# Kernel optimization log

Hardware: AMD Instinct MI355X
Metric: run time of the kernel (lower is better)

## Reference

```python
import jax, jax.numpy as jnp
import numpy as np

NUM_USERS = 100000
NUM_ITEMS = 100000
D = 64
L = 3
B = 4096
K = 50


def setup_inputs() -> dict:
    key = jax.random.key(0)
    ks = jax.random.split(key, 8)
    user_ids = jax.random.randint(ks[0], (B,), 0, NUM_USERS)
    item_ids = jax.random.randint(ks[1], (B,), 0, NUM_ITEMS)
    social_neighbors = jax.random.randint(ks[2], (B, K), 0, NUM_USERS)
    attention_mask = jax.random.uniform(ks[3], (B, K), dtype=jnp.float32)
    user_table = jax.random.normal(ks[4], (NUM_USERS, D), dtype=jnp.float32) * 0.1
    item_table = jax.random.normal(ks[5], (NUM_ITEMS, D), dtype=jnp.float32) * 0.1
    # xavier-ish scale for the square Linear layers
    Ws = jax.random.normal(ks[6], (L, D, D), dtype=jnp.float32) * (1.0 / np.sqrt(D))
    bs = jnp.zeros((L, D), dtype=jnp.float32)
    return {
        "user_ids": user_ids,
        "item_ids": item_ids,
        "social_neighbors": social_neighbors,
        "attention_mask": attention_mask,
        "user_table": user_table,
        "item_table": item_table,
        "Ws": Ws,
        "bs": bs,
    }


def reference(user_ids, item_ids, social_neighbors, attention_mask,
              user_table, item_table, Ws, bs):
    user_emb = user_table[user_ids]            # [B, D]
    item_emb = item_table[item_ids]            # [B, D]
    neighbor_emb = user_table[social_neighbors]  # [B, K, D]
    mask = attention_mask[..., None]           # [B, K, 1]
    for l in range(Ws.shape[0]):
        # faithful to original: mask is re-applied to neighbor_emb every layer
        neighbor_emb = neighbor_emb * mask
        neighbor_info = jnp.mean(neighbor_emb, axis=1)  # [B, D]
        # nn.Linear: x @ W.T + b
        user_emb = jax.nn.relu((user_emb + neighbor_info) @ Ws[l].T + bs[l])
    scores = user_emb @ item_emb.T              # [B, B]
    return scores
```

## Files before the change

kernel.cpp:

```cpp
#include <hip/hip_runtime.h>
#include <hip/hip_bf16.h>

#define BATCH 4096
#define DIM 64
#define KN 50
#define NL 3

typedef __attribute__((ext_vector_type(8))) short short8;
typedef __attribute__((ext_vector_type(4))) float f32x4;

__global__ __launch_bounds__(256) void rows_kernel(
    const int* __restrict__ user_ids,
    const int* __restrict__ item_ids,
    const int* __restrict__ nbrs,
    const float* __restrict__ mask,
    const float* __restrict__ user_table,
    const float* __restrict__ item_table,
    const float* __restrict__ Ws,
    const float* __restrict__ bs,
    __hip_bfloat16* __restrict__ Uout,
    __hip_bfloat16* __restrict__ Iout)
{
    __shared__ float Wlds[NL * 64 * 65];
    __shared__ float blds[NL * 64];
    __shared__ float xbuf[4][64];

    const int tid = threadIdx.x;

    for (int idx = tid; idx < NL * 64 * 64; idx += 256) {
        const int l = idx >> 12;
        const int rem = idx & 4095;
        const int j = rem >> 6;
        const int i = rem & 63;
        Wlds[l * (64 * 65) + j * 65 + i] = Ws[idx];
    }
    if (tid < NL * 64) blds[tid] = bs[tid];
    __syncthreads();

    const int wave = tid >> 6;
    const int lane = tid & 63;
    const int b = (blockIdx.x << 2) + wave;

    const int it = item_ids[b];
    Iout[b * DIM + lane] = __float2bfloat16(item_table[it * DIM + lane]);

    const int u = user_ids[b];
    float x = user_table[u * DIM + lane];

    int ni = 0;
    float wi = 0.0f;
    if (lane < KN) {
        ni = nbrs[b * KN + lane];
        wi = mask[b * KN + lane];
    }

    float acc1 = 0.f, acc2 = 0.f, acc3 = 0.f;
    #pragma unroll
    for (int k = 0; k < KN; ++k) {
        const int nk = __shfl(ni, k);
        const float wk = __shfl(wi, k);
        const float v = user_table[nk * DIM + lane];
        const float w2 = wk * wk;
        acc1 = fmaf(wk, v, acc1);
        acc2 = fmaf(w2, v, acc2);
        acc3 = fmaf(w2 * wk, v, acc3);
    }
    const float inv = 1.0f / (float)KN;
    const float nm0 = acc1 * inv, nm1 = acc2 * inv, nm2 = acc3 * inv;

    #pragma unroll
    for (int l = 0; l < NL; ++l) {
        const float nm = (l == 0) ? nm0 : (l == 1) ? nm1 : nm2;
        xbuf[wave][lane] = x + nm;
        float y = blds[l * 64 + lane];
        const float* wrow = &Wlds[l * (64 * 65) + lane * 65];
        #pragma unroll
        for (int i = 0; i < 64; ++i)
            y = fmaf(wrow[i], xbuf[wave][i], y);
        x = fmaxf(y, 0.0f);
    }
    Uout[b * DIM + lane] = __float2bfloat16(x);
}

__global__ __launch_bounds__(256) void scores_kernel(
    const __hip_bfloat16* __restrict__ U,
    const __hip_bfloat16* __restrict__ V,
    float* __restrict__ C)
{
    const int tid = threadIdx.x;
    const int wave = tid >> 6;
    const int lane = tid & 63;
    const int quad = lane >> 4;
    const int l16 = lane & 15;

    const int row0 = (blockIdx.y << 6) + (wave << 4);
    const int colG = blockIdx.x << 8;

    const short* Us = (const short*)U;
    const short* Vs = (const short*)V;

    const short* up = Us + (row0 + l16) * DIM + quad * 8;
    const short8 u0 = *(const short8*)(up);
    const short8 u1 = *(const short8*)(up + 32);

    #pragma unroll 4
    for (int ct = 0; ct < 16; ++ct) {
        const int col0 = colG + (ct << 4);
        const short* vp = Vs + (col0 + l16) * DIM + quad * 8;
        const short8 v0 = *(const short8*)(vp);
        const short8 v1 = *(const short8*)(vp + 32);
        f32x4 acc = {0.f, 0.f, 0.f, 0.f};
        acc = __builtin_amdgcn_mfma_f32_16x16x32_bf16(v0, u0, acc, 0, 0, 0);
        acc = __builtin_amdgcn_mfma_f32_16x16x32_bf16(v1, u1, acc, 0, 0, 0);
        float* cp = C + (size_t)(row0 + l16) * BATCH + col0 + (quad << 2);
        *(float4*)cp = make_float4(acc[0], acc[1], acc[2], acc[3]);
    }
}

extern "C" void kernel_launch(void* const* d_in, const int* in_sizes, int n_in,
                              void* d_out, int out_size, void* d_ws, size_t ws_size,
                              hipStream_t stream)
{
    const int* user_ids   = (const int*)d_in[0];
    const int* item_ids   = (const int*)d_in[1];
    const int* nbrs       = (const int*)d_in[2];
    const float* mask     = (const float*)d_in[3];
    const float* utable   = (const float*)d_in[4];
    const float* itable   = (const float*)d_in[5];
    const float* Ws       = (const float*)d_in[6];
    const float* bs       = (const float*)d_in[7];
    float* out = (float*)d_out;

    __hip_bfloat16* Ubf = (__hip_bfloat16*)d_ws;
    __hip_bfloat16* Ibf = Ubf + BATCH * DIM;

    rows_kernel<<<BATCH / 4, 256, 0, stream>>>(user_ids, item_ids, nbrs, mask,
                                               utable, itable, Ws, bs, Ubf, Ibf);
    scores_kernel<<<dim3(16, 64), 256, 0, stream>>>(Ubf, Ibf, out);
}
```

Baseline: 142.2 us.

## Split gather from MLP and amortize weight LDS loads over four rows

Measured after the change: 139.8 us. Within noise of the previous version (-1.7%).

```diff
diff --git a/kernel.cpp b/kernel.cpp
--- a/kernel.cpp
+++ b/kernel.cpp
@@ -9,21 +9,60 @@
 typedef __attribute__((ext_vector_type(8))) short short8;
 typedef __attribute__((ext_vector_type(4))) float f32x4;
 
-__global__ __launch_bounds__(256) void rows_kernel(
+__global__ __launch_bounds__(256) void gather_kernel(
     const int* __restrict__ user_ids,
     const int* __restrict__ item_ids,
     const int* __restrict__ nbrs,
     const float* __restrict__ mask,
     const float* __restrict__ user_table,
     const float* __restrict__ item_table,
+    float* __restrict__ X0,
+    float* __restrict__ NM1,
+    float* __restrict__ NM2,
+    __hip_bfloat16* __restrict__ Iout)
+{
+    const int tid = threadIdx.x;
+    const int wave = tid >> 6;
+    const int lane = tid & 63;
+    const int b = __builtin_amdgcn_readfirstlane((blockIdx.x << 2) + wave);
+
+    const int it = item_ids[b];
+    Iout[b * DIM + lane] = __float2bfloat16(item_table[it * DIM + lane]);
+
+    const int u = user_ids[b];
+    const float x = user_table[u * DIM + lane];
+
+    const int* __restrict__ nrow = nbrs + b * KN;
+    const float* __restrict__ mrow = mask + b * KN;
+
+    float acc1 = 0.f, acc2 = 0.f, acc3 = 0.f;
+    #pragma unroll
+    for (int k = 0; k < KN; ++k) {
+        const int nk = nrow[k];
+        const float wk = mrow[k];
+        const float v = user_table[nk * DIM + lane];
+        const float w2 = wk * wk;
+        acc1 = fmaf(wk, v, acc1);
+        acc2 = fmaf(w2, v, acc2);
+        acc3 = fmaf(w2 * wk, v, acc3);
+    }
+    const float inv = 1.0f / (float)KN;
+    X0[b * DIM + lane]  = x + acc1 * inv;
+    NM1[b * DIM + lane] = acc2 * inv;
+    NM2[b * DIM + lane] = acc3 * inv;
+}
+
+__global__ __launch_bounds__(256) void mlp_kernel(
+    const float* __restrict__ X0,
+    const float* __restrict__ NM1,
+    const float* __restrict__ NM2,
     const float* __restrict__ Ws,
     const float* __restrict__ bs,
-    __hip_bfloat16* __restrict__ Uout,
-    __hip_bfloat16* __restrict__ Iout)
+    __hip_bfloat16* __restrict__ Uout)
 {
     __shared__ float Wlds[NL * 64 * 65];
     __shared__ float blds[NL * 64];
-    __shared__ float xbuf[4][64];
+    __shared__ float4 xb[4][64];
 
     const int tid = threadIdx.x;
 
@@ -39,47 +78,42 @@
 
     const int wave = tid >> 6;
     const int lane = tid & 63;
-    const int b = (blockIdx.x << 2) + wave;
+    const int r0 = (blockIdx.x << 4) + (wave << 2);
 
-    const int it = item_ids[b];
-    Iout[b * DIM + lane] = __float2bfloat16(item_table[it * DIM + lane]);
-
-    const int u = user_ids[b];
-    float x = user_table[u * DIM + lane];
-
-    int ni = 0;
-    float wi = 0.0f;
-    if (lane < KN) {
-        ni = nbrs[b * KN + lane];
-        wi = mask[b * KN + lane];
-    }
-
-    float acc1 = 0.f, acc2 = 0.f, acc3 = 0.f;
-    #pragma unroll
-    for (int k = 0; k < KN; ++k) {
-        const int nk = __shfl(ni, k);
-        const float wk = __shfl(wi, k);
-        const float v = user_table[nk * DIM + lane];
-        const float w2 = wk * wk;
-        acc1 = fmaf(wk, v, acc1);
-        acc2 = fmaf(w2, v, acc2);
-        acc3 = fmaf(w2 * wk, v, acc3);
-    }
-    const float inv = 1.0f / (float)KN;
-    const float nm0 = acc1 * inv, nm1 = acc2 * inv, nm2 = acc3 * inv;
+    float x0 = X0[(r0 + 0) * DIM + lane];
+    float x1 = X0[(r0 + 1) * DIM + lane];
+    float x2 = X0[(r0 + 2) * DIM + lane];
+    float x3 = X0[(r0 + 3) * DIM + lane];
 
     #pragma unroll
     for (int l = 0; l < NL; ++l) {
-        const float nm = (l == 0) ? nm0 : (l == 1) ? nm1 : nm2;
-        xbuf[wave][lane] = x + nm;
-        float y = blds[l * 64 + lane];
+        xb[wave][lane] = make_float4(x0, x1, x2, x3);
+        float y0 = blds[l * 64 + lane], y1 = y0, y2 = y0, y3 = y0;
         const float* wrow = &Wlds[l * (64 * 65) + lane * 65];
         #pragma unroll
-        for (int i = 0; i < 64; ++i)
-            y = fmaf(wrow[i], xbuf[wave][i], y);
-        x = fmaxf(y, 0.0f);
+        for (int i = 0; i < 64; ++i) {
+            const float w = wrow[i];
+            const float4 xv = xb[wave][i];
+            y0 = fmaf(w, xv.x, y0);
+            y1 = fmaf(w, xv.y, y1);
+            y2 = fmaf(w, xv.z, y2);
+            y3 = fmaf(w, xv.w, y3);
+        }
+        if (l < NL - 1) {
+            const float* NM = (l == 0) ? NM1 : NM2;
+            x0 = fmaxf(y0, 0.f) + NM[(r0 + 0) * DIM + lane];
+            x1 = fmaxf(y1, 0.f) + NM[(r0 + 1) * DIM + lane];
+            x2 = fmaxf(y2, 0.f) + NM[(r0 + 2) * DIM + lane];
+            x3 = fmaxf(y3, 0.f) + NM[(r0 + 3) * DIM + lane];
+        } else {
+            x0 = fmaxf(y0, 0.f); x1 = fmaxf(y1, 0.f);
+            x2 = fmaxf(y2, 0.f); x3 = fmaxf(y3, 0.f);
+        }
     }
-    Uout[b * DIM + lane] = __float2bfloat16(x);
+    Uout[(r0 + 0) * DIM + lane] = __float2bfloat16(x0);
+    Uout[(r0 + 1) * DIM + lane] = __float2bfloat16(x1);
+    Uout[(r0 + 2) * DIM + lane] = __float2bfloat16(x2);
+    Uout[(r0 + 3) * DIM + lane] = __float2bfloat16(x3);
 }
 
 __global__ __launch_bounds__(256) void scores_kernel(
@@ -131,10 +165,14 @@
     const float* bs       = (const float*)d_in[7];
     float* out = (float*)d_out;
 
-    __hip_bfloat16* Ubf = (__hip_bfloat16*)d_ws;
+    float* X0  = (float*)d_ws;
+    float* NM1 = X0 + BATCH * DIM;
+    float* NM2 = NM1 + BATCH * DIM;
+    __hip_bfloat16* Ubf = (__hip_bfloat16*)(NM2 + BATCH * DIM);
     __hip_bfloat16* Ibf = Ubf + BATCH * DIM;
 
-    rows_kernel<<<BATCH / 4, 256, 0, stream>>>(user_ids, item_ids, nbrs, mask,
-                                               utable, itable, Ws, bs, Ubf, Ibf);
+    gather_kernel<<<BATCH / 4, 256, 0, stream>>>(user_ids, item_ids, nbrs, mask,
+                                                 utable, itable, X0, NM1, NM2, Ibf);
+    mlp_kernel<<<BATCH / 16, 256, 0, stream>>>(X0, NM1, NM2, Ws, bs, Ubf);
     scores_kernel<<<dim3(16, 64), 256, 0, stream>>>(Ubf, Ibf, out);
 }
```

## Process four rows per wave in gather/MLP kernel and use nontemporal score stores

Applied to the files above, without the earlier changes.

Measured after the change: 143.2 us. Within noise of the previous version (+0.7%).

```diff
diff --git a/kernel.cpp b/kernel.cpp
--- a/kernel.cpp
+++ b/kernel.cpp
@@ -9,7 +9,7 @@
 typedef __attribute__((ext_vector_type(8))) short short8;
 typedef __attribute__((ext_vector_type(4))) float f32x4;
 
-__global__ __launch_bounds__(256) void rows_kernel(
+__global__ __launch_bounds__(256) void gather_mlp_kernel(
     const int* __restrict__ user_ids,
     const int* __restrict__ item_ids,
     const int* __restrict__ nbrs,
@@ -23,7 +23,7 @@
 {
     __shared__ float Wlds[NL * 64 * 65];
     __shared__ float blds[NL * 64];
-    __shared__ float xbuf[4][64];
+    __shared__ float4 xb[4][64];
 
     const int tid = threadIdx.x;
 
@@ -39,47 +39,69 @@
 
     const int wave = tid >> 6;
     const int lane = tid & 63;
-    const int b = (blockIdx.x << 2) + wave;
+    const int r0 = __builtin_amdgcn_readfirstlane((blockIdx.x << 4) + (wave << 2));
 
-    const int it = item_ids[b];
-    Iout[b * DIM + lane] = __float2bfloat16(item_table[it * DIM + lane]);
+    float x[4], nm1[4], nm2[4];
 
-    const int u = user_ids[b];
-    float x = user_table[u * DIM + lane];
+    #pragma unroll
+    for (int r = 0; r < 4; ++r) {
+        const int b = r0 + r;
 
-    int ni = 0;
-    float wi = 0.0f;
-    if (lane < KN) {
-        ni = nbrs[b * KN + lane];
-        wi = mask[b * KN + lane];
+        const int it = item_ids[b];
+        Iout[b * DIM + lane] = __float2bfloat16(item_table[it * DIM + lane]);
+
+        const int u = user_ids[b];
+        const float ue = user_table[u * DIM + lane];
+
+        const int* __restrict__ nrow = nbrs + b * KN;
+        const float* __restrict__ mrow = mask + b * KN;
+
+        float acc1 = 0.f, acc2 = 0.f, acc3 = 0.f;
+        #pragma unroll
+        for (int k = 0; k < KN; ++k) {
+            const int nk = nrow[k];
+            const float wk = mrow[k];
+            const float v = user_table[nk * DIM + lane];
+            const float w2 = wk * wk;
+            acc1 = fmaf(wk, v, acc1);
+            acc2 = fmaf(w2, v, acc2);
+            acc3 = fmaf(w2 * wk, v, acc3);
+        }
+        const float inv = 1.0f / (float)KN;
+        x[r]   = ue + acc1 * inv;
+        nm1[r] = acc2 * inv;
+        nm2[r] = acc3 * inv;
     }
-
-    float acc1 = 0.f, acc2 = 0.f, acc3 = 0.f;
-    #pragma unroll
-    for (int k = 0; k < KN; ++k) {
-        const int nk = __shfl(ni, k);
-        const float wk = __shfl(wi, k);
-        const float v = user_table[nk * DIM + lane];
-        const float w2 = wk * wk;
-        acc1 = fmaf(wk, v, acc1);
-        acc2 = fmaf(w2, v, acc2);
-        acc3 = fmaf(w2 * wk, v, acc3);
-    }
-    const float inv = 1.0f / (float)KN;
-    const float nm0 = acc1 * inv, nm1 = acc2 * inv, nm2 = acc3 * inv;
 
     #pragma unroll
     for (int l = 0; l < NL; ++l) {
-        const float nm = (l == 0) ? nm0 : (l == 1) ? nm1 : nm2;
-        xbuf[wave][lane] = x + nm;
-        float y = blds[l * 64 + lane];
+        xb[wave][lane] = make_float4(x[0], x[1], x[2], x[3]);
+        float y0 = blds[l * 64 + lane], y1 = y0, y2 = y0, y3 = y0;
         const float* wrow = &Wlds[l * (64 * 65) + lane * 65];
         #pragma unroll
-        for (int i = 0; i < 64; ++i)
-            y = fmaf(wrow[i], xbuf[wave][i], y);
-        x = fmaxf(y, 0.0f);
+        for (int i = 0; i < 64; ++i) {
+            const float w = wrow[i];
+            const float4 xv = xb[wave][i];
+            y0 = fmaf(w, xv.x, y0);
+            y1 = fmaf(w, xv.y, y1);
+            y2 = fmaf(w, xv.z, y2);
+            y3 = fmaf(w, xv.w, y3);
+        }
+        if (l == 0) {
+            x[0] = fmaxf(y0, 0.f) + nm1[0]; x[1] = fmaxf(y1, 0.f) + nm1[1];
+            x[2] = fmaxf(y2, 0.f) + nm1[2]; x[3] = fmaxf(y3, 0.f) + nm1[3];
+        } else if (l == 1) {
+            x[0] = fmaxf(y0, 0.f) + nm2[0]; x[1] = fmaxf(y1, 0.f) + nm2[1];
+            x[2] = fmaxf(y2, 0.f) + nm2[2]; x[3] = fmaxf(y3, 0.f) + nm2[3];
+        } else {
+            x[0] = fmaxf(y0, 0.f); x[1] = fmaxf(y1, 0.f);
+            x[2] = fmaxf(y2, 0.f); x[3] = fmaxf(y3, 0.f);
+        }
     }
-    Uout[b * DIM + lane] = __float2bfloat16(x);
+    Uout[(r0 + 0) * DIM + lane] = __float2bfloat16(x[0]);
+    Uout[(r0 + 1) * DIM + lane] = __float2bfloat16(x[1]);
+    Uout[(r0 + 2) * DIM + lane] = __float2bfloat16(x[2]);
+    Uout[(r0 + 3) * DIM + lane] = __float2bfloat16(x[3]);
 }
 
 __global__ __launch_bounds__(256) void scores_kernel(
@@ -112,8 +134,8 @@
         f32x4 acc = {0.f, 0.f, 0.f, 0.f};
         acc = __builtin_amdgcn_mfma_f32_16x16x32_bf16(v0, u0, acc, 0, 0, 0);
         acc = __builtin_amdgcn_mfma_f32_16x16x32_bf16(v1, u1, acc, 0, 0, 0);
-        float* cp = C + (size_t)(row0 + l16) * BATCH + col0 + (quad << 2);
-        *(float4*)cp = make_float4(acc[0], acc[1], acc[2], acc[3]);
+        f32x4* cp = (f32x4*)(C + (size_t)(row0 + l16) * BATCH + col0 + (quad << 2));
+        __builtin_nontemporal_store(acc, cp);
     }
 }
 
@@ -134,7 +156,8 @@
     __hip_bfloat16* Ubf = (__hip_bfloat16*)d_ws;
     __hip_bfloat16* Ibf = Ubf + BATCH * DIM;
 
-    rows_kernel<<<BATCH / 4, 256, 0, stream>>>(user_ids, item_ids, nbrs, mask,
-                                               utable, itable, Ws, bs, Ubf, Ibf);
+    gather_mlp_kernel<<<BATCH / 16, 256, 0, stream>>>(user_ids, item_ids, nbrs,
+                                                      mask, utable, itable, Ws, bs,
+                                                      Ubf, Ibf);
     scores_kernel<<<dim3(16, 64), 256, 0, stream>>>(Ubf, Ibf, out);
 }
```
